# Kernel optimization log

Measured on AMD Instinct MI355X. Metric: run time of the kernel, lower is better.

Reference implementation:

```python
import jax, jax.numpy as jnp
import numpy as np

EMBED_SIZE = 1024
HEADS = 16
HEAD_DIM = EMBED_SIZE // HEADS  # 64


def setup_inputs() -> dict:
    key = jax.random.key(0)
    k_x, k_q, k_k, k_v, k_o, k_b = jax.random.split(key, 6)
    B, S = 32, 8192  # S divisible by HEADS
    x = jax.random.normal(k_x, (B, S, HEAD_DIM), dtype=jnp.float32)
    # torch.nn.Linear weights are [out, in]; scale ~ 1/sqrt(fan_in)
    s_h = 1.0 / np.sqrt(HEAD_DIM)
    s_e = 1.0 / np.sqrt(EMBED_SIZE)
    Wq = jax.random.uniform(k_q, (HEAD_DIM, HEAD_DIM), jnp.float32, -s_h, s_h)
    Wk = jax.random.uniform(k_k, (HEAD_DIM, HEAD_DIM), jnp.float32, -s_h, s_h)
    Wv = jax.random.uniform(k_v, (HEAD_DIM, HEAD_DIM), jnp.float32, -s_h, s_h)
    Wo = jax.random.uniform(k_o, (EMBED_SIZE, EMBED_SIZE), jnp.float32, -s_e, s_e)
    bo = jax.random.uniform(k_b, (EMBED_SIZE,), jnp.float32, -s_e, s_e)
    return {"x": x, "Wq": Wq, "Wk": Wk, "Wv": Wv, "Wo": Wo, "bo": bo}


def reference(x, Wq, Wk, Wv, Wo, bo):
    B = x.shape[0]
    # Q/K/V projections: Linear(head_dim, head_dim), bias=False -> x @ W.T
    Q = (x @ Wq.T).reshape(B, -1, HEADS, HEAD_DIM)  # [B, G, H, D], G = S/H
    K = (x @ Wk.T).reshape(B, -1, HEADS, HEAD_DIM)
    V = (x @ Wv.T).reshape(B, -1, HEADS, HEAD_DIM)
    # energy = Q @ K^T over last two dims -> [B, G, H, H]
    energy = jnp.einsum('bghd,bgkd->bghk', Q, K)
    attn = jax.nn.softmax(energy / jnp.sqrt(jnp.float32(EMBED_SIZE)), axis=3)
    out = jnp.einsum('bghk,bgkd->bghd', attn, V)      # [B, G, H, D]
    out = out.transpose(0, 2, 1, 3).reshape(B, -1, EMBED_SIZE)  # [B, S/H, E]
    return out @ Wo.T + bo
```

## Files before the change

### kernel.cpp

```cpp
#include <hip/hip_runtime.h>
#include <hip/hip_bf16.h>
#include <stdint.h>

#define TOKS   262144
#define NGRP   16384
#define EMB    1024
#define HD     64

using bf16x8 = __attribute__((ext_vector_type(8))) short;
using f32x4  = __attribute__((ext_vector_type(4))) float;

__device__ __forceinline__ unsigned pack2(float a, float b) {
    union { __hip_bfloat162 h; unsigned u; } cvt;
    cvt.h = __float22bfloat162_rn(make_float2(a, b));
    return cvt.u;
}
__device__ __forceinline__ bf16x8 cvt8(float4 v0, float4 v1) {
    uint4 u;
    u.x = pack2(v0.x, v0.y);
    u.y = pack2(v0.z, v0.w);
    u.z = pack2(v1.x, v1.y);
    u.w = pack2(v1.z, v1.w);
    return __builtin_bit_cast(bf16x8, u);
}
__device__ __forceinline__ int swz(int r) {
    return ((r ^ (r >> 2) ^ (r >> 4)) & 7) << 3;
}

__global__ __launch_bounds__(256) void k_cvt(const float* __restrict__ wo,
                                             const float* __restrict__ wq,
                                             const float* __restrict__ wk,
                                             const float* __restrict__ wv,
                                             unsigned short* __restrict__ wob,
                                             unsigned short* __restrict__ wqkvb) {
    int bid = blockIdx.x;
    if (bid < 512) {
        int tid = bid * 256 + threadIdx.x;
        int kc  = tid >> 12;
        int nb  = (tid >> 6) & 63;
        int l   = tid & 63;
        int n   = nb * 16 + (l & 15);
        int k   = kc * 32 + (l >> 4) * 8;
        const float* src = wo + (size_t)n * 1024 + k;
        float4 v0 = *(const float4*)(src);
        float4 v1 = *(const float4*)(src + 4);
        *(bf16x8*)(wob + (size_t)tid * 8) = cvt8(v0, v1);
    } else {
        int b = bid - 512;
        int m = b >> 2;
        const float* src = (m == 0) ? wq : ((m == 1) ? wk : wv);
        int idx = ((b & 3) * 256 + threadIdx.x) * 4;
        float4 v = *(const float4*)(src + idx);
        uint2 p;
        p.x = pack2(v.x, v.y);
        p.y = pack2(v.z, v.w);
        *(uint2*)(wqkvb + m * 4096 + idx) = p;
    }
}

#define SCL 0.0450842200278f

#define MFMA_B16(A, B, Cc) __builtin_amdgcn_mfma_f32_16x16x32_bf16(A, B, Cc, 0, 0, 0)

__global__ __launch_bounds__(512, 2) void k_mega(const float* __restrict__ x,
                                                 const unsigned short* __restrict__ wqkv,
                                                 const unsigned short* __restrict__ wob,
                                                 const float* __restrict__ bias,
                                                 float* __restrict__ C) {
    extern __shared__ __align__(16) unsigned short lds[];
    unsigned short* out2s = lds;
    unsigned short* kscr  = lds + 65536;

    const int t = threadIdx.x;
    const int w = t >> 6, l = t & 63;
    const int c = l & 15, q = l >> 4;
    const int bid   = blockIdx.x;
    const int batch = bid >> 3, q8 = bid & 3 + 0, q8r = bid & 7;
    unsigned short* kw = kscr + w * 1024;

    const int gbq = w >> 1;
    const int gc0 = (w & 1) * 8;

    const int mS0 = swz(16 * q + gbq);
    const int mS1 = swz(16 * q + gbq + 4);
    const int mS2 = swz(16 * q + gbq + 8);
    const int mS3 = swz(16 * q + gbq + 12);
    const int mkw = swz(c);
    const int mqe = swz(c * 4 + gbq);
    const int mk0 = swz(4 * q);
    const int mk1 = swz(4 * q + 1);
    const int mk2 = swz(4 * q + 2);
    const int mk3 = swz(4 * q + 3);

    const float* xb = x + ((size_t)bid * 1024 + c) * 64 + q * 8;

    float4 xr[2][4];
    #pragma unroll
    for (int g = 0; g < 2; ++g) {
        const float* xp = xb + (size_t)(w * 8 + g) * 1024;
        xr[g][0] = *(const float4*)(xp);
        xr[g][1] = *(const float4*)(xp + 4);
        xr[g][2] = *(const float4*)(xp + 32);
        xr[g][3] = *(const float4*)(xp + 36);
    }

    #pragma unroll 1
    for (int p = 0; p < 4; ++p) {
        bf16x8 xa[2][2];
        #pragma unroll
        for (int g = 0; g < 2; ++g) {
            xa[g][0] = cvt8(xr[g][0], xr[g][1]);
            xa[g][1] = cvt8(xr[g][2], xr[g][3]);
        }
        if (p < 3) {
            #pragma unroll
            for (int g = 0; g < 2; ++g) {
                const float* xp = xb + (size_t)(w * 8 + 2 * (p + 1) + g) * 1024;
                xr[g][0] = *(const float4*)(xp);
                xr[g][1] = *(const float4*)(xp + 4);
                xr[g][2] = *(const float4*)(xp + 32);
                xr[g][3] = *(const float4*)(xp + 36);
            }
        }

        unsigned short* qs[2];
        qs[0] = out2s + (size_t)(16 * q + gbq) * 1024 + (gc0 + 2 * p) * 64;
        qs[1] = qs[0] + 64;

        #pragma unroll
        for (int nb = 0; nb < 4; ++nb) {
            const unsigned short* wp = wqkv + (nb * 16 + c) * 64 + q * 8;
            bf16x8 w0 = *(const bf16x8*)(wp);
            bf16x8 w1 = *(const bf16x8*)(wp + 32);
            #pragma unroll
            for (int g = 0; g < 2; ++g) {
                f32x4 acc = (f32x4){0.f, 0.f, 0.f, 0.f};
                acc = MFMA_B16(xa[g][0], w0, acc);
                acc = MFMA_B16(xa[g][1], w1, acc);
                unsigned u01 = pack2(acc[0], acc[1]);
                unsigned u23 = pack2(acc[2], acc[3]);
                const int d = nb * 16 + c;
                qs[g][(d ^ mS0)]             = (unsigned short)u01;
                qs[g][4 * 1024 + (d ^ mS1)]  = (unsigned short)(u01 >> 16);
                qs[g][8 * 1024 + (d ^ mS2)]  = (unsigned short)u23;
                qs[g][12 * 1024 + (d ^ mS3)] = (unsigned short)(u23 >> 16);
            }
        }

        uint2 pkV[2][4];
        #pragma unroll
        for (int nb = 0; nb < 4; ++nb) {
            const unsigned short* wp = wqkv + 2 * 4096 + (nb * 16 + c) * 64 + q * 8;
            bf16x8 w0 = *(const bf16x8*)(wp);
            bf16x8 w1 = *(const bf16x8*)(wp + 32);
            #pragma unroll
            for (int g = 0; g < 2; ++g) {
                f32x4 acc = (f32x4){0.f, 0.f, 0.f, 0.f};
                acc = MFMA_B16(xa[g][0], w0, acc);
                acc = MFMA_B16(xa[g][1], w1, acc);
                pkV[g][nb].x = pack2(acc[0], acc[1]);
                pkV[g][nb].y = pack2(acc[2], acc[3]);
            }
        }

        f32x4 e[2];
        #pragma unroll
        for (int g = 0; g < 2; ++g) {
            #pragma unroll
            for (int nb = 0; nb < 4; ++nb) {
                const unsigned short* wp = wqkv + 4096 + (nb * 16 + c) * 64 + q * 8;
                bf16x8 w0 = *(const bf16x8*)(wp);
                bf16x8 w1 = *(const bf16x8*)(wp + 32);
                f32x4 acc = (f32x4){0.f, 0.f, 0.f, 0.f};
                acc = MFMA_B16(xa[g][0], w0, acc);
                acc = MFMA_B16(xa[g][1], w1, acc);
                unsigned u01 = pack2(acc[0], acc[1]);
                unsigned u23 = pack2(acc[2], acc[3]);
                const int d = nb * 16 + c;
                const int kr = 4 * q;
                kw[(kr + 0) * 64 + (d ^ mk0)] = (unsigned short)u01;
                kw[(kr + 1) * 64 + (d ^ mk1)] = (unsigned short)(u01 >> 16);
                kw[(kr + 2) * 64 + (d ^ mk2)] = (unsigned short)u23;
                kw[(kr + 3) * 64 + (d ^ mk3)] = (unsigned short)(u23 >> 16);
            }
            e[g] = (f32x4){0.f, 0.f, 0.f, 0.f};
            const unsigned short* qrow = out2s + (size_t)(c * 4 + gbq) * 1024
                                               + (gc0 + 2 * p + g) * 64;
            #pragma unroll
            for (int kc2 = 0; kc2 < 2; ++kc2) {
                const int L = kc2 * 32 + q * 8;
                bf16x8 ka = *(const bf16x8*)(kw + c * 64 + (L ^ mkw));
                bf16x8 qb = *(const bf16x8*)(qrow + (L ^ mqe));
                e[g] = MFMA_B16(ka, qb, e[g]);
            }
        }

        unsigned pa0[2], pa1[2];
        #pragma unroll
        for (int g = 0; g < 2; ++g) {
            float mx = fmaxf(fmaxf(e[g][0], e[g][1]), fmaxf(e[g][2], e[g][3]));
            mx = fmaxf(mx, __shfl_xor(mx, 16));
            mx = fmaxf(mx, __shfl_xor(mx, 32));
            float p0 = exp2f((e[g][0] - mx) * SCL);
            float p1 = exp2f((e[g][1] - mx) * SCL);
            float p2 = exp2f((e[g][2] - mx) * SCL);
            float p3 = exp2f((e[g][3] - mx) * SCL);
            float s = p0 + p1 + p2 + p3;
            s += __shfl_xor(s, 16);
            s += __shfl_xor(s, 32);
            float rinv = 1.0f / s;
            pa0[g] = pack2(p0 * rinv, p1 * rinv);
            pa1[g] = pack2(p2 * rinv, p3 * rinv);
        }

        const int sh0 = (32 * q + c) & 63;
        const int sh1 = (32 * q + 16 + c) & 63;
        const int sv0 = 32 * (q & 1) + c;
        const int sv1 = sv0 + 16;
        const bool hi = (q >= 2);
        #pragma unroll
        for (int g = 0; g < 2; ++g) {
            int a0 = __shfl((int)pa0[g], sh0);
            int a1 = __shfl((int)pa1[g], sh0);
            int a2 = __shfl((int)pa0[g], sh1);
            int a3 = __shfl((int)pa1[g], sh1);
            uint4 A2u;
            A2u.x = hi ? 0u : (unsigned)a0;
            A2u.y = hi ? 0u : (unsigned)a1;
            A2u.z = hi ? 0u : (unsigned)a2;
            A2u.w = hi ? 0u : (unsigned)a3;
            bf16x8 A2 = __builtin_bit_cast(bf16x8, A2u);

            #pragma unroll
            for (int nb = 0; nb < 4; ++nb) {
                uint4 B2u;
                B2u.x = (unsigned)__shfl((int)pkV[g][nb].x, sv0);
                B2u.y = (unsigned)__shfl((int)pkV[g][nb].y, sv0);
                B2u.z = (unsigned)__shfl((int)pkV[g][nb].x, sv1);
                B2u.w = (unsigned)__shfl((int)pkV[g][nb].y, sv1);
                bf16x8 B2 = __builtin_bit_cast(bf16x8, B2u);
                f32x4 o = (f32x4){0.f, 0.f, 0.f, 0.f};
                o = MFMA_B16(A2, B2, o);
                unsigned u01 = pack2(o[0], o[1]);
                unsigned u23 = pack2(o[2], o[3]);
                const int d = nb * 16 + c;
                qs[g][(d ^ mS0)]             = (unsigned short)u01;
                qs[g][4 * 1024 + (d ^ mS1)]  = (unsigned short)(u01 >> 16);
                qs[g][8 * 1024 + (d ^ mS2)]  = (unsigned short)u23;
                qs[g][12 * 1024 + (d ^ mS3)] = (unsigned short)(u23 >> 16);
            }
        }
    }

    __syncthreads();

    const unsigned short* gBw = wob + (size_t)(w * 8) * 512 + (size_t)l * 8;
    float bc[8];
    #pragma unroll
    for (int nb = 0; nb < 8; ++nb) bc[nb] = bias[w * 128 + nb * 16 + c];

    f32x4 acc[4][8];
    #pragma unroll
    for (int m = 0; m < 4; ++m)
        #pragma unroll
        for (int nb = 0; nb < 8; ++nb)
            acc[m][nb] = (f32x4){0.f, 0.f, 0.f, 0.f};

    bf16x8 bE[8], bO[8], a[4];

    #pragma unroll
    for (int nb = 0; nb < 8; ++nb) bE[nb] = *(const bf16x8*)(gBw + nb * 512);

    #pragma unroll 1
    for (int tt = 0; tt < 16; ++tt) {
        const size_t kb = (size_t)tt * 65536;
        #pragma unroll
        for (int nb = 0; nb < 8; ++nb)
            bO[nb] = *(const bf16x8*)(gBw + kb + 32768 + nb * 512);
        {
            const int L = (2 * tt) * 32 + q * 8;
            #pragma unroll
            for (int m = 0; m < 4; ++m)
                a[m] = *(const bf16x8*)(out2s + (size_t)(m * 16 + c) * 1024
                                              + (L ^ swz(m * 16 + c)));
            #pragma unroll
            for (int m = 0; m < 4; ++m)
                #pragma unroll
                for (int nb = 0; nb < 8; ++nb)
                    acc[m][nb] = MFMA_B16(a[m], bE[nb], acc[m][nb]);
        }
        if (tt < 15) {
            #pragma unroll
            for (int nb = 0; nb < 8; ++nb)
                bE[nb] = *(const bf16x8*)(gBw + kb + 65536 + nb * 512);
        }
        {
            const int L = (2 * tt + 1) * 32 + q * 8;
            #pragma unroll
            for (int m = 0; m < 4; ++m)
                a[m] = *(const bf16x8*)(out2s + (size_t)(m * 16 + c) * 1024
                                              + (L ^ swz(m * 16 + c)));
            #pragma unroll
            for (int m = 0; m < 4; ++m)
                #pragma unroll
                for (int nb = 0; nb < 8; ++nb)
                    acc[m][nb] = MFMA_B16(a[m], bO[nb], acc[m][nb]);
        }
    }

    #pragma unroll
    for (int m = 0; m < 4; ++m) {
        #pragma unroll
        for (int r = 0; r < 4; ++r) {
            const int rg = batch * 512 + (m * 4 + q) * 32 + q8r * 4 + r;
            float* cp = C + (size_t)rg * 1024 + w * 128 + c;
            #pragma unroll
            for (int nb = 0; nb < 8; ++nb)
                cp[nb * 16] = acc[m][nb][r] + bc[nb];
        }
    }
}

extern "C" void kernel_launch(void* const* d_in, const int* in_sizes, int n_in,
                              void* d_out, int out_size, void* d_ws, size_t ws_size,
                              hipStream_t stream) {
    const float* x  = (const float*)d_in[0];
    const float* wq = (const float*)d_in[1];
    const float* wk = (const float*)d_in[2];
    const float* wv = (const float*)d_in[3];
    const float* wo = (const float*)d_in[4];
    const float* bo = (const float*)d_in[5];
    float* out = (float*)d_out;

    unsigned short* wob   = (unsigned short*)d_ws;
    unsigned short* wqkvb = wob + (size_t)EMB * EMB;

    static int s_once = []() {
        hipFuncSetAttribute((const void*)k_mega,
                            hipFuncAttributeMaxDynamicSharedMemorySize, 147456);
        return 0;
    }();
    (void)s_once;

    k_cvt <<<524, 256, 0, stream>>>(wo, wq, wk, wv, wob, wqkvb);
    k_mega<<<256, 512, 147456, stream>>>(x, wqkvb, wob, bo, out);
}
```

Baseline: 151.5 us.

## Interleave output-projection GEMM chunks with attention pair processing per warp group

Splits the final Wo GEMM into four K-chunks, and runs chunk p-1 in the same loop iteration as attention pair p, separated by a barrier each iteration. Half the warps do the GEMM chunk first and the other half do attention first, so MFMA-heavy and LDS/global-heavy phases overlap across waves. The change drops the register prefetch of x and the double-buffered Wo loads, and keeps the 128-float accumulator array live through the attention phase. That raises register pressure and may cause spills or lower occupancy.

```diff
diff --git a/kernel.cpp b/kernel.cpp
--- a/kernel.cpp
+++ b/kernel.cpp
@@ -75,7 +75,7 @@
     const int w = t >> 6, l = t & 63;
     const int c = l & 15, q = l >> 4;
     const int bid   = blockIdx.x;
-    const int batch = bid >> 3, q8 = bid & 3 + 0, q8r = bid & 7;
+    const int batch = bid >> 3, q8r = bid & 7;
     unsigned short* kw = kscr + w * 1024;
 
     const int gbq = w >> 1;
@@ -93,34 +93,30 @@
     const int mk3 = swz(4 * q + 3);
 
     const float* xb = x + ((size_t)bid * 1024 + c) * 64 + q * 8;
-
-    float4 xr[2][4];
+    const unsigned short* gBw = wob + (size_t)(w * 8) * 512 + (size_t)l * 8;
+
+    f32x4 acc[4][8];
     #pragma unroll
-    for (int g = 0; g < 2; ++g) {
-        const float* xp = xb + (size_t)(w * 8 + g) * 1024;
-        xr[g][0] = *(const float4*)(xp);
-        xr[g][1] = *(const float4*)(xp + 4);
-        xr[g][2] = *(const float4*)(xp + 32);
-        xr[g][3] = *(const float4*)(xp + 36);
-    }
-
-    #pragma unroll 1
-    for (int p = 0; p < 4; ++p) {
+    for (int m = 0; m < 4; ++m)
+        #pragma unroll
+        for (int nb = 0; nb < 8; ++nb)
+            acc[m][nb] = (f32x4){0.f, 0.f, 0.f, 0.f};
+
+    auto PAIR = [&](int p) {
+        float4 xr[2][4];
+        #pragma unroll
+        for (int g = 0; g < 2; ++g) {
+            const float* xp = xb + (size_t)(w * 8 + 2 * p + g) * 1024;
+            xr[g][0] = *(const float4*)(xp);
+            xr[g][1] = *(const float4*)(xp + 4);
+            xr[g][2] = *(const float4*)(xp + 32);
+            xr[g][3] = *(const float4*)(xp + 36);
+        }
         bf16x8 xa[2][2];
         #pragma unroll
         for (int g = 0; g < 2; ++g) {
             xa[g][0] = cvt8(xr[g][0], xr[g][1]);
             xa[g][1] = cvt8(xr[g][2], xr[g][3]);
-        }
-        if (p < 3) {
-            #pragma unroll
-            for (int g = 0; g < 2; ++g) {
-                const float* xp = xb + (size_t)(w * 8 + 2 * (p + 1) + g) * 1024;
-                xr[g][0] = *(const float4*)(xp);
-                xr[g][1] = *(const float4*)(xp + 4);
-                xr[g][2] = *(const float4*)(xp + 32);
-                xr[g][3] = *(const float4*)(xp + 36);
-            }
         }
 
         unsigned short* qs[2];
@@ -134,11 +130,11 @@
             bf16x8 w1 = *(const bf16x8*)(wp + 32);
             #pragma unroll
             for (int g = 0; g < 2; ++g) {
-                f32x4 acc = (f32x4){0.f, 0.f, 0.f, 0.f};
-                acc = MFMA_B16(xa[g][0], w0, acc);
-                acc = MFMA_B16(xa[g][1], w1, acc);
-                unsigned u01 = pack2(acc[0], acc[1]);
-                unsigned u23 = pack2(acc[2], acc[3]);
+                f32x4 a2 = (f32x4){0.f, 0.f, 0.f, 0.f};
+                a2 = MFMA_B16(xa[g][0], w0, a2);
+                a2 = MFMA_B16(xa[g][1], w1, a2);
+                unsigned u01 = pack2(a2[0], a2[1]);
+                unsigned u23 = pack2(a2[2], a2[3]);
                 const int d = nb * 16 + c;
                 qs[g][(d ^ mS0)]             = (unsigned short)u01;
                 qs[g][4 * 1024 + (d ^ mS1)]  = (unsigned short)(u01 >> 16);
@@ -155,11 +151,11 @@
             bf16x8 w1 = *(const bf16x8*)(wp + 32);
             #pragma unroll
             for (int g = 0; g < 2; ++g) {
-                f32x4 acc = (f32x4){0.f, 0.f, 0.f, 0.f};
-                acc = MFMA_B16(xa[g][0], w0, acc);
-                acc = MFMA_B16(xa[g][1], w1, acc);
-                pkV[g][nb].x = pack2(acc[0], acc[1]);
-                pkV[g][nb].y = pack2(acc[2], acc[3]);
+                f32x4 a2 = (f32x4){0.f, 0.f, 0.f, 0.f};
+                a2 = MFMA_B16(xa[g][0], w0, a2);
+                a2 = MFMA_B16(xa[g][1], w1, a2);
+                pkV[g][nb].x = pack2(a2[0], a2[1]);
+                pkV[g][nb].y = pack2(a2[2], a2[3]);
             }
         }
 
@@ -171,11 +167,11 @@
                 const unsigned short* wp = wqkv + 4096 + (nb * 16 + c) * 64 + q * 8;
                 bf16x8 w0 = *(const bf16x8*)(wp);
                 bf16x8 w1 = *(const bf16x8*)(wp + 32);
-                f32x4 acc = (f32x4){0.f, 0.f, 0.f, 0.f};
-                acc = MFMA_B16(xa[g][0], w0, acc);
-                acc = MFMA_B16(xa[g][1], w1, acc);
-                unsigned u01 = pack2(acc[0], acc[1]);
-                unsigned u23 = pack2(acc[2], acc[3]);
+                f32x4 a2 = (f32x4){0.f, 0.f, 0.f, 0.f};
+                a2 = MFMA_B16(xa[g][0], w0, a2);
+                a2 = MFMA_B16(xa[g][1], w1, a2);
+                unsigned u01 = pack2(a2[0], a2[1]);
+                unsigned u23 = pack2(a2[2], a2[3]);
                 const int d = nb * 16 + c;
                 const int kr = 4 * q;
                 kw[(kr + 0) * 64 + (d ^ mk0)] = (unsigned short)u01;
@@ -250,73 +246,59 @@
                 qs[g][12 * 1024 + (d ^ mS3)] = (unsigned short)(u23 >> 16);
             }
         }
+    };
+
+    auto CHUNK = [&](int cp) {
+        #pragma unroll
+        for (int h = 0; h < 2; ++h) {
+            #pragma unroll
+            for (int kk = 0; kk < 4; ++kk) {
+                const int kc = h * 16 + 4 * cp + kk;
+                bf16x8 bb[8];
+                #pragma unroll
+                for (int nb = 0; nb < 8; ++nb)
+                    bb[nb] = *(const bf16x8*)(gBw + (size_t)kc * 32768 + nb * 512);
+                const int L = kc * 32 + q * 8;
+                bf16x8 av[4];
+                #pragma unroll
+                for (int m = 0; m < 4; ++m)
+                    av[m] = *(const bf16x8*)(out2s + (size_t)(m * 16 + c) * 1024
+                                                   + (L ^ swz(m * 16 + c)));
+                #pragma unroll
+                for (int m = 0; m < 4; ++m)
+                    #pragma unroll
+                    for (int nb = 0; nb < 8; ++nb)
+                        acc[m][nb] = MFMA_B16(av[m], bb[nb], acc[m][nb]);
+            }
+        }
+    };
+
+    #pragma unroll 1
+    for (int p = 0; p < 4; ++p) {
+        __syncthreads();
+        if (w >= 4) {
+            if (p > 0) CHUNK(p - 1);
+            PAIR(p);
+        } else {
+            PAIR(p);
+            if (p > 0) CHUNK(p - 1);
+        }
     }
-
     __syncthreads();
-
-    const unsigned short* gBw = wob + (size_t)(w * 8) * 512 + (size_t)l * 8;
+    CHUNK(3);
+
     float bc[8];
     #pragma unroll
     for (int nb = 0; nb < 8; ++nb) bc[nb] = bias[w * 128 + nb * 16 + c];
-
-    f32x4 acc[4][8];
-    #pragma unroll
-    for (int m = 0; m < 4; ++m)
-        #pragma unroll
-        for (int nb = 0; nb < 8; ++nb)
-            acc[m][nb] = (f32x4){0.f, 0.f, 0.f, 0.f};
-
-    bf16x8 bE[8], bO[8], a[4];
-
-    #pragma unroll
-    for (int nb = 0; nb < 8; ++nb) bE[nb] = *(const bf16x8*)(gBw + nb * 512);
-
-    #pragma unroll 1
-    for (int tt = 0; tt < 16; ++tt) {
-        const size_t kb = (size_t)tt * 65536;
-        #pragma unroll
-        for (int nb = 0; nb < 8; ++nb)
-            bO[nb] = *(const bf16x8*)(gBw + kb + 32768 + nb * 512);
-        {
-            const int L = (2 * tt) * 32 + q * 8;
-            #pragma unroll
-            for (int m = 0; m < 4; ++m)
-                a[m] = *(const bf16x8*)(out2s + (size_t)(m * 16 + c) * 1024
-                                              + (L ^ swz(m * 16 + c)));
-            #pragma unroll
-            for (int m = 0; m < 4; ++m)
-                #pragma unroll
-                for (int nb = 0; nb < 8; ++nb)
-                    acc[m][nb] = MFMA_B16(a[m], bE[nb], acc[m][nb]);
-        }
-        if (tt < 15) {
-            #pragma unroll
-            for (int nb = 0; nb < 8; ++nb)
-                bE[nb] = *(const bf16x8*)(gBw + kb + 65536 + nb * 512);
-        }
-        {
-            const int L = (2 * tt + 1) * 32 + q * 8;
-            #pragma unroll
-            for (int m = 0; m < 4; ++m)
-                a[m] = *(const bf16x8*)(out2s + (size_t)(m * 16 + c) * 1024
-                                              + (L ^ swz(m * 16 + c)));
-            #pragma unroll
-            for (int m = 0; m < 4; ++m)
-                #pragma unroll
-                for (int nb = 0; nb < 8; ++nb)
-                    acc[m][nb] = MFMA_B16(a[m], bO[nb], acc[m][nb]);
-        }
-    }
-
     #pragma unroll
     for (int m = 0; m < 4; ++m) {
         #pragma unroll
         for (int r = 0; r < 4; ++r) {
             const int rg = batch * 512 + (m * 4 + q) * 32 + q8r * 4 + r;
-            float* cp = C + (size_t)rg * 1024 + w * 128 + c;
+            float* cp2 = C + (size_t)rg * 1024 + w * 128 + c;
             #pragma unroll
             for (int nb = 0; nb < 8; ++nb)
-                cp[nb * 16] = acc[m][nb][r] + bc[nb];
+                cp2[nb * 16] = acc[m][nb][r] + bc[nb];
         }
     }
 }
```

Result: slower. 207.7 us (+37.1%).
